# Kernel tuning notes

Hardware: AMD Instinct MI355X
Metric: run time of the kernel (lower is better)

## Reference

```python
import jax, jax.numpy as jnp
import numpy as np

HEADS = 4
DIM_HEAD = 64
SCALE = 8.0
EPS = 1e-5  # fp32 branch of the original LayerNorm


def setup_inputs() -> dict:
    key = jax.random.key(0)
    k1, k2, k3 = jax.random.split(key, 3)
    B, C, F, H, W = 2, 256, 4, 32, 32
    inner = HEADS * DIM_HEAD  # 256
    x = jax.random.normal(k1, (B, C, F, H, W), dtype=jnp.float32)
    gamma = jnp.ones((1, C, 1, 1, 1), dtype=jnp.float32)
    w_qkv = jax.random.normal(k2, (3 * inner, C), dtype=jnp.float32) * 0.05
    w_out = jax.random.normal(k3, (C, inner), dtype=jnp.float32) * 0.05
    return {"x": x, "gamma": gamma, "w_qkv": w_qkv, "w_out": w_out}


def _l2norm(t):
    return t / jnp.sqrt(jnp.sum(t * t, axis=-1, keepdims=True) + 1e-12)


def reference(x, gamma, w_qkv, w_out):
    B, C, F, H, W = x.shape
    N = F * H * W
    inner = HEADS * DIM_HEAD
    residual = x

    # channel LayerNorm (biased variance over dim=1)
    mean = jnp.mean(x, axis=1, keepdims=True)
    var = jnp.mean((x - mean) ** 2, axis=1, keepdims=True)
    xn = (x - mean) / jnp.sqrt(var + EPS) * gamma

    # 1x1x1 conv == channel matmul; flatten spatial dims to sequence
    xn_flat = xn.reshape(B, C, N)                      # [B, C, N]
    qkv = jnp.einsum('oc,bcn->bon', w_qkv, xn_flat)    # [B, 3*inner, N]
    qkv = qkv.reshape(B, 3, HEADS, DIM_HEAD, N)        # chunk then split heads
    qkv = jnp.transpose(qkv, (1, 0, 2, 4, 3))          # [3, B, h, N, d]
    q, k, v = qkv[0], qkv[1], qkv[2]

    q = _l2norm(q)
    k = _l2norm(k)

    sim = jnp.einsum('bhid,bhjd->bhij', q, k) * SCALE  # [B, h, N, N]
    attn = jax.nn.softmax(sim, axis=-1)
    out = jnp.einsum('bhij,bhjd->bhid', attn, v)       # [B, h, N, d]

    # 'b h n d -> b (h d) n' then 1x1x1 out conv
    out = jnp.transpose(out, (0, 1, 3, 2)).reshape(B, inner, N)
    out = jnp.einsum('oi,bin->bon', w_out, out).reshape(B, C, F, H, W)
    return out + residual
```

## Files before the change

kernel.cpp:

```cpp
#include <hip/hip_runtime.h>

#define BATCH 2
#define CCH   256
#define NSEQ  4096
#define NH    4
#define DH    64
#define INNER 256

typedef __attribute__((ext_vector_type(8))) __bf16 bf16x8;
typedef __attribute__((ext_vector_type(4))) float f32x4;
typedef __attribute__((ext_vector_type(8))) unsigned short u16x8;
typedef __attribute__((ext_vector_type(4))) unsigned short u16x4;

#define GLD16(gsrc, ldst)                                                     \
  __builtin_amdgcn_global_load_lds(                                           \
      (const __attribute__((address_space(1))) unsigned int*)(const void*)(gsrc), \
      (__attribute__((address_space(3))) unsigned int*)(void*)(ldst), 16, 0, 0)

static __device__ __forceinline__ unsigned short f2bfr(float f) {
  union { float f; unsigned u; } v; v.f = f;
  return (unsigned short)((v.u + 0x8000u) >> 16);
}
static __device__ __forceinline__ unsigned pack2(float f0, float f1) {
  union { float f; unsigned u; } a, b; a.f = f0; b.f = f1;
  return __builtin_amdgcn_perm(b.u + 0x8000u, a.u + 0x8000u, 0x07060302u);
}
static __device__ __forceinline__ unsigned cvtpk(float lo, float hi) {
  unsigned r;
  asm("v_cvt_pk_bf16_f32 %0, %1, %2" : "=v"(r) : "v"(lo), "v"(hi));
  return r;
}
static __device__ __forceinline__ float bf2f(unsigned short u) {
  union { unsigned u; float f; } v; v.u = ((unsigned)u) << 16;
  return v.f;
}
static __device__ __forceinline__ bf16x8 ldb(const unsigned short* p) {
  return *(const bf16x8*)p;
}
static __device__ __forceinline__ f32x4 mm(bf16x8 a, bf16x8 b, f32x4 c) {
  return __builtin_amdgcn_mfma_f32_16x16x32_bf16(a, b, c, 0, 0, 0);
}
static __device__ __forceinline__ float ex2(float x) {
  return __builtin_amdgcn_exp2f(x);
}

__global__ __launch_bounds__(256) void k_lncvt(const float* __restrict__ x,
                                               const float* __restrict__ gamma,
                                               unsigned short* __restrict__ xn,
                                               const float* __restrict__ wq,
                                               const float* __restrict__ wo,
                                               unsigned short* __restrict__ wqb,
                                               unsigned short* __restrict__ wob) {
  int blk = blockIdx.x;
  if (blk >= 256) {
    int t = (blk - 256) * 256 + threadIdx.x;
    int e = t * 4;
    if (e < 768 * 256) {
      float4 v = *(const float4*)(wq + e);
      u16x4 pk = { f2bfr(v.x), f2bfr(v.y), f2bfr(v.z), f2bfr(v.w) };
      *(u16x4*)(wqb + e) = pk;
    } else {
      int e2 = e - 768 * 256;
      float4 v = *(const float4*)(wo + e2);
      u16x4 pk = { f2bfr(v.x), f2bfr(v.y), f2bfr(v.z), f2bfr(v.w) };
      *(u16x4*)(wob + e2) = pk;
    }
    return;
  }
  int b  = blk >> 7;
  int n0 = (blk & 127) * 32;
  int t  = threadIdx.x;
  int nl = t & 31;
  int cg = t >> 5;
  int n  = n0 + nl;
  const float* xp = x + ((size_t)(b * CCH + cg * 32)) * NSEQ + n;
  float vals[32];
  float s = 0.f, s2 = 0.f;
#pragma unroll
  for (int j = 0; j < 32; j++) {
    float v = xp[(size_t)j * NSEQ];
    vals[j] = v; s += v; s2 += v * v;
  }
  __shared__ float rs[8][32], rs2[8][32];
  rs[cg][nl] = s; rs2[cg][nl] = s2;
  __syncthreads();
  float S = 0.f, S2 = 0.f;
#pragma unroll
  for (int g = 0; g < 8; g++) { S += rs[g][nl]; S2 += rs2[g][nl]; }
  float mean = S * (1.f / 256.f);
  float var  = S2 * (1.f / 256.f) - mean * mean;
  float rstd = rsqrtf(var + 1e-5f);
  unsigned short* dst = xn + ((size_t)b * NSEQ + n) * CCH + cg * 32;
#pragma unroll
  for (int j0 = 0; j0 < 32; j0 += 8) {
    u16x8 pk;
#pragma unroll
    for (int j = 0; j < 8; j++)
      pk[j] = f2bfr((vals[j0 + j] - mean) * rstd * gamma[cg * 32 + j0 + j]);
    *(u16x8*)(dst + j0) = pk;
  }
}

__global__ __launch_bounds__(256) void k_qkv(const unsigned short* __restrict__ wqb,
                                             const unsigned short* __restrict__ xn,
                                             unsigned short* __restrict__ qkv,
                                             unsigned short* __restrict__ qt,
                                             unsigned short* __restrict__ ktb) {
  int n0 = blockIdx.x * 64;
  int oi = blockIdx.y;
  int o0 = oi * 64;
  int b  = blockIdx.z;
  __shared__ unsigned short Al[64 * 256];
  __shared__ unsigned short Bl[64 * 256];
  int t = threadIdx.x;
  int lane = t & 63, w = t >> 6;
  int c = lane & 15, quad = lane >> 4;
  int wm = w >> 1, wn = w & 1;
  f32x4 acc[2][2] = {};
  int lr2 = lane >> 5;
  int lch = lane & 31;
  const unsigned short* apg = wqb + (size_t)o0 * CCH;
  const unsigned short* bpg = xn + ((size_t)b * NSEQ + n0) * CCH;
#pragma unroll
  for (int q = 0; q < 8; q++) {
    int r = w * 16 + q * 2 + lr2;
    int srcoff = r * CCH + ((lch ^ (r & 7)) * 8);
    GLD16(apg + srcoff, Al + (size_t)(w * 16 + q * 2) * 256);
    GLD16(bpg + srcoff, Bl + (size_t)(w * 16 + q * 2) * 256);
  }
  __syncthreads();
#pragma unroll
  for (int ks = 0; ks < 8; ks++) {
    int ra0 = wm * 32 + c, ra1 = ra0 + 16;
    int rb0 = wn * 32 + c, rb1 = rb0 + 16;
    bf16x8 a0 = ldb(&Al[ra0 * 256 + (((ks * 4 + quad) ^ (ra0 & 7)) * 8)]);
    bf16x8 a1 = ldb(&Al[ra1 * 256 + (((ks * 4 + quad) ^ (ra1 & 7)) * 8)]);
    bf16x8 b0 = ldb(&Bl[rb0 * 256 + (((ks * 4 + quad) ^ (rb0 & 7)) * 8)]);
    bf16x8 b1 = ldb(&Bl[rb1 * 256 + (((ks * 4 + quad) ^ (rb1 & 7)) * 8)]);
    acc[0][0] = mm(a0, b0, acc[0][0]);
    acc[0][1] = mm(a0, b1, acc[0][1]);
    acc[1][0] = mm(a1, b0, acc[1][0]);
    acc[1][1] = mm(a1, b1, acc[1][1]);
  }
  if (oi < 8) {
    float* sq = (float*)Al;
    float s0 = 0.f, s1 = 0.f;
#pragma unroll
    for (int i = 0; i < 2; i++)
#pragma unroll
      for (int rr = 0; rr < 4; rr++) {
        s0 += acc[i][0][rr] * acc[i][0][rr];
        s1 += acc[i][1][rr] * acc[i][1][rr];
      }
    s0 += __shfl_xor(s0, 16); s0 += __shfl_xor(s0, 32);
    s1 += __shfl_xor(s1, 16); s1 += __shfl_xor(s1, 32);
    __syncthreads();
    if (quad == 0) {
      sq[wm * 64 + wn * 32 + c]      = s0;
      sq[wm * 64 + wn * 32 + 16 + c] = s1;
    }
    __syncthreads();
    float r0 = rsqrtf(sq[wn * 32 + c]      + sq[64 + wn * 32 + c]      + 1e-12f);
    float r1 = rsqrtf(sq[wn * 32 + 16 + c] + sq[64 + wn * 32 + 16 + c] + 1e-12f);
    if (oi < 4) { r0 *= 11.541560327111707f; r1 *= 11.541560327111707f; }
    int h = oi & 3;
    unsigned short* base = (oi < 4 ? qt : ktb) + ((size_t)(b * NH + h) * NSEQ) * DH;
#pragma unroll
    for (int i = 0; i < 2; i++)
#pragma unroll
      for (int j = 0; j < 2; j++) {
        float rsc = j ? r1 : r0;
        int n = n0 + wn * 32 + j * 16 + c;
        int d = wm * 32 + i * 16 + quad * 4;
        uint2 pk = { pack2(acc[i][j][0] * rsc, acc[i][j][1] * rsc),
                     pack2(acc[i][j][2] * rsc, acc[i][j][3] * rsc) };
        *(uint2*)(base + (size_t)n * DH + d) = pk;
      }
  } else {
#pragma unroll
    for (int i = 0; i < 2; i++)
#pragma unroll
      for (int j = 0; j < 2; j++)
#pragma unroll
        for (int rr = 0; rr < 4; rr++) {
          int o = o0 + wm * 32 + i * 16 + quad * 4 + rr;
          int n = n0 + wn * 32 + j * 16 + c;
          qkv[((size_t)b * 768 + o) * NSEQ + n] = f2bfr(acc[i][j][rr]);
        }
  }
}

__global__ __launch_bounds__(256, 4) void k_attn(
    const unsigned short* __restrict__ qt,
    const unsigned short* __restrict__ ktb,
    const unsigned short* __restrict__ qkv,
    unsigned short* __restrict__ opart,
    float* __restrict__ lpart,
    int S, int kvlen) {
  int i0 = blockIdx.x * 128;
  int h  = blockIdx.y;
  int bz = blockIdx.z;
  int b  = bz / S, s = bz % S;
  __shared__ unsigned short Kl[64 * 64];
  __shared__ unsigned short Vl[2][64 * 64];
  __shared__ unsigned short Pl[128 * 64];
  int t = threadIdx.x;
  int lane = t & 63, w = t >> 6;
  int c = lane & 15, quad = lane >> 4;

  const unsigned short* qbase = qt  + ((size_t)(b * NH + h) * NSEQ) * DH;
  const unsigned short* kbase = ktb + ((size_t)(b * NH + h) * NSEQ) * DH;
  const unsigned short* vbase = qkv + ((size_t)b * 768 + 512 + h * 64) * NSEQ;

  int rlo = w * 32 + c, rhi = rlo + 16;
  const unsigned short* qlo = qbase + (size_t)(i0 + rlo) * DH + quad * 8;
  const unsigned short* qhi = qlo + 16 * DH;
  bf16x8 qlo0 = ldb(qlo), qlo1 = ldb(qlo + 32);
  bf16x8 qhi0 = ldb(qhi), qhi1 = ldb(qhi + 32);

  u16x8 onesu;
#pragma unroll
  for (int j = 0; j < 8; j++) onesu[j] = 0x3F80;
  bf16x8 ones = *(bf16x8*)&onesu;

  f32x4 acclo[4] = {}, acchi[4] = {};
  f32x4 accllo = {}, acclhi = {};

  int slr = lane >> 3, slc = lane & 7;
  int ssw = (slc ^ slr) * 8;
  const unsigned short* kp = kbase + (size_t)(s * kvlen + w * 16 + slr) * DH + ssw;
  const unsigned short* vp = vbase + (size_t)(w * 16 + slr) * NSEQ + s * kvlen + ssw;
  int sw0 = (quad ^ (c & 7)) * 8;
  int sw1 = sw0 ^ 32;
  int r7 = rlo & 7;

  int nIt = kvlen / 64;
  GLD16(kp,            &Kl[(w * 16)     * 64]);
  GLD16(kp + 8 * DH,   &Kl[(w * 16 + 8) * 64]);
  GLD16(vp,            &Vl[0][(w * 16)     * 64]);
  GLD16(vp + 8 * NSEQ, &Vl[0][(w * 16 + 8) * 64]);
  kp += 64 * DH; vp += 64;

  for (int it = 0; it < nIt; it++) {
    int cur = it & 1;
    __syncthreads();
    if (it + 1 < nIt) {
      int nb = cur ^ 1;
      GLD16(vp,            &Vl[nb][(w * 16)     * 64]);
      GLD16(vp + 8 * NSEQ, &Vl[nb][(w * 16 + 8) * 64]);
      vp += 64;
    }

#pragma unroll
    for (int jt = 0; jt < 4; jt++) {
      bf16x8 k0 = ldb(&Kl[(jt * 16 + c) * 64 + sw0]);
      bf16x8 k1 = ldb(&Kl[(jt * 16 + c) * 64 + sw1]);
      __builtin_amdgcn_s_setprio(1);
      f32x4 zl = {}; zl = mm(k0, qlo0, zl); zl = mm(k1, qlo1, zl);
      f32x4 zh = {}; zh = mm(k0, qhi0, zh); zh = mm(k1, qhi1, zh);
      __builtin_amdgcn_s_setprio(0);
      int cj = jt * 2 + (quad >> 1);
      int sub = (quad & 1) * 4;
      uint2 pkl = { cvtpk(ex2(zl[0]), ex2(zl[1])),
                    cvtpk(ex2(zl[2]), ex2(zl[3])) };
      *(uint2*)&Pl[rlo * 64 + ((cj ^ r7) * 8) + sub] = pkl;
      uint2 pkh = { cvtpk(ex2(zh[0]), ex2(zh[1])),
                    cvtpk(ex2(zh[2]), ex2(zh[3])) };
      *(uint2*)&Pl[rhi * 64 + ((cj ^ r7) * 8) + sub] = pkh;
    }
    bf16x8 plo0 = ldb(&Pl[rlo * 64 + ((quad ^ r7) * 8)]);
    bf16x8 plo1 = ldb(&Pl[rlo * 64 + (((quad + 4) ^ r7) * 8)]);
    bf16x8 phi0 = ldb(&Pl[rhi * 64 + ((quad ^ r7) * 8)]);
    bf16x8 phi1 = ldb(&Pl[rhi * 64 + (((quad + 4) ^ r7) * 8)]);

    if (it + 1 < nIt) {
      __builtin_amdgcn_sched_barrier(0);
      __builtin_amdgcn_s_barrier();
      __builtin_amdgcn_sched_barrier(0);
      GLD16(kp,          &Kl[(w * 16)     * 64]);
      GLD16(kp + 8 * DH, &Kl[(w * 16 + 8) * 64]);
      kp += 64 * DH;
    }

#pragma unroll
    for (int dt = 0; dt < 4; dt++) {
      bf16x8 v0 = ldb(&Vl[cur][(dt * 16 + c) * 64 + sw0]);
      bf16x8 v1 = ldb(&Vl[cur][(dt * 16 + c) * 64 + sw1]);
      __builtin_amdgcn_s_setprio(1);
      acclo[dt] = mm(plo0, v0, acclo[dt]);
      acclo[dt] = mm(plo1, v1, acclo[dt]);
      acchi[dt] = mm(phi0, v0, acchi[dt]);
      acchi[dt] = mm(phi1, v1, acchi[dt]);
      __builtin_amdgcn_s_setprio(0);
    }
    __builtin_amdgcn_s_setprio(1);
    accllo = mm(plo0, ones, accllo); accllo = mm(plo1, ones, accllo);
    acclhi = mm(phi0, ones, acclhi); acclhi = mm(phi1, ones, acclhi);
    __builtin_amdgcn_s_setprio(0);
  }

  size_t rb = ((size_t)(b * NH + h) * S + s) * NSEQ + i0 + w * 32;
  if (c == 0) {
#pragma unroll
    for (int rr = 0; rr < 4; rr++) {
      lpart[rb + quad * 4 + rr]      = accllo[rr];
      lpart[rb + 16 + quad * 4 + rr] = acclhi[rr];
    }
  }
#pragma unroll
  for (int rr = 0; rr < 4; rr++)
#pragma unroll
    for (int dt = 0; dt < 4; dt++) {
      opart[(rb + quad * 4 + rr) * 64 + dt * 16 + c]      = f2bfr(acclo[dt][rr]);
      opart[(rb + 16 + quad * 4 + rr) * 64 + dt * 16 + c] = f2bfr(acchi[dt][rr]);
    }
}

__global__ __launch_bounds__(256) void k_merge(
    const unsigned short* __restrict__ opart,
    const float* __restrict__ lpart,
    unsigned short* __restrict__ ao, int S) {
  int t = blockIdx.x * 256 + threadIdx.x;
  int row = t >> 2;
  int dseg = (t & 3) * 16;
  int b = row >> 14, rem = row & 16383;
  int h = rem >> 12, i = rem & 4095;

  float l = 0.f;
  float o[16];
#pragma unroll
  for (int j = 0; j < 16; j++) o[j] = 0.f;
  for (int s = 0; s < S; s++) {
    size_t rb = ((size_t)(b * NH + h) * S + s) * NSEQ + i;
    l += lpart[rb];
    const unsigned short* p = opart + rb * 64 + dseg;
    u16x8 v0 = *(const u16x8*)p;
    u16x8 v1 = *(const u16x8*)(p + 8);
#pragma unroll
    for (int j = 0; j < 8; j++) {
      o[j]     += bf2f(v0[j]);
      o[8 + j] += bf2f(v1[j]);
    }
  }
  float inv = 1.f / l;
  unsigned short* dst = ao + ((size_t)b * NSEQ + i) * INNER + h * 64 + dseg;
  uint4 pk0 = { pack2(o[0] * inv, o[1] * inv),  pack2(o[2] * inv, o[3] * inv),
                pack2(o[4] * inv, o[5] * inv),  pack2(o[6] * inv, o[7] * inv) };
  uint4 pk1 = { pack2(o[8] * inv, o[9] * inv),  pack2(o[10] * inv, o[11] * inv),
                pack2(o[12] * inv, o[13] * inv),pack2(o[14] * inv, o[15] * inv) };
  *(uint4*)dst = pk0;
  *(uint4*)(dst + 8) = pk1;
}

__global__ __launch_bounds__(256) void k_out(const unsigned short* __restrict__ wob,
                                             const unsigned short* __restrict__ ao,
                                             const float* __restrict__ x,
                                             float* __restrict__ out) {
  int n0 = blockIdx.x * 64;
  int o0 = blockIdx.y * 64;
  int b  = blockIdx.z;
  __shared__ unsigned short Al[64 * 256];
  __shared__ unsigned short Bl[64 * 256];
  int t = threadIdx.x;
  int lane = t & 63, w = t >> 6;
  int c = lane & 15, quad = lane >> 4;
  int wm = w >> 1, wn = w & 1;
  f32x4 acc[2][2] = {};
  int lr2 = lane >> 5;
  int lch = lane & 31;
  const unsigned short* apg = wob + (size_t)o0 * INNER;
  const unsigned short* bpg = ao + ((size_t)b * NSEQ + n0) * INNER;
#pragma unroll
  for (int q = 0; q < 8; q++) {
    int r = w * 16 + q * 2 + lr2;
    int srcoff = r * INNER + ((lch ^ (r & 7)) * 8);
    GLD16(apg + srcoff, Al + (size_t)(w * 16 + q * 2) * 256);
    GLD16(bpg + srcoff, Bl + (size_t)(w * 16 + q * 2) * 256);
  }
  __syncthreads();
#pragma unroll
  for (int ks = 0; ks < 8; ks++) {
    int ra0 = wm * 32 + c, ra1 = ra0 + 16;
    int rb0 = wn * 32 + c, rb1 = rb0 + 16;
    bf16x8 a0 = ldb(&Al[ra0 * 256 + (((ks * 4 + quad) ^ (ra0 & 7)) * 8)]);
    bf16x8 a1 = ldb(&Al[ra1 * 256 + (((ks * 4 + quad) ^ (ra1 & 7)) * 8)]);
    bf16x8 b0 = ldb(&Bl[rb0 * 256 + (((ks * 4 + quad) ^ (rb0 & 7)) * 8)]);
    bf16x8 b1 = ldb(&Bl[rb1 * 256 + (((ks * 4 + quad) ^ (rb1 & 7)) * 8)]);
    acc[0][0] = mm(a0, b0, acc[0][0]);
    acc[0][1] = mm(a0, b1, acc[0][1]);
    acc[1][0] = mm(a1, b0, acc[1][0]);
    acc[1][1] = mm(a1, b1, acc[1][1]);
  }
#pragma unroll
  for (int i = 0; i < 2; i++)
#pragma unroll
    for (int j = 0; j < 2; j++)
#pragma unroll
      for (int rr = 0; rr < 4; rr++) {
        int o = o0 + wm * 32 + i * 16 + quad * 4 + rr;
        int n = n0 + wn * 32 + j * 16 + c;
        size_t idx = ((size_t)b * CCH + o) * NSEQ + n;
        out[idx] = acc[i][j][rr] + x[idx];
      }
}

extern "C" void kernel_launch(void* const* d_in, const int* in_sizes, int n_in,
                              void* d_out, int out_size, void* d_ws, size_t ws_size,
                              hipStream_t stream) {
  const float* x     = (const float*)d_in[0];
  const float* gamma = (const float*)d_in[1];
  const float* wq    = (const float*)d_in[2];
  const float* wo    = (const float*)d_in[3];
  float* out = (float*)d_out;

  const size_t MB = 1u << 20;
  char* ws = (char*)d_ws;
  unsigned short* ao  = (unsigned short*)ws;
  unsigned short* xn  = (unsigned short*)(ws + 4 * MB);
  unsigned short* qkv = (unsigned short*)(ws + 8 * MB);
  unsigned short* wqb = (unsigned short*)(ws + 20 * MB);
  unsigned short* wob = (unsigned short*)(ws + 20 * MB + 512 * 1024);
  unsigned short* qt  = (unsigned short*)(ws + 21 * MB);
  unsigned short* ktb = (unsigned short*)(ws + 25 * MB);
  unsigned short* opart = (unsigned short*)(ws + 29 * MB);
  int S;
  if (ws_size >= 48 * MB) S = 4;
  else if (ws_size >= 40 * MB) S = 2;
  else S = 1;
  size_t opart_bytes = (size_t)S * BATCH * NH * NSEQ * DH * 2;
  float* lpart = (float*)(ws + 29 * MB + opart_bytes);
  int kvlen = NSEQ / S;

  k_lncvt<<<dim3(512),          256, 0, stream>>>(x, gamma, xn, wq, wo, wqb, wob);
  k_qkv  <<<dim3(64, 12, 2),    256, 0, stream>>>(wqb, xn, qkv, qt, ktb);
  k_attn <<<dim3(32, 4, 2 * S), 256, 0, stream>>>(qt, ktb, qkv, opart,
                                                  lpart, S, kvlen);
  k_merge<<<dim3(512),          256, 0, stream>>>(opart, lpart, ao, S);
  k_out  <<<dim3(64, 4, 2),     256, 0, stream>>>(wob, ao, x, out);
}
```

Before: 128.9 us.

## Keep attention probabilities in registers by permuting K rows to match MFMA layout

The attention kernel now loads K tiles straight from global memory into registers, using a permuted row mapping so the QK^T MFMA output lands in the operand layout the PV MFMA needs. This removes the shared-memory P buffer, its round trip, the K shared tile and one block barrier per iteration. In exchange every wave loads K from global memory itself with no sharing in LDS, which adds global/L2 traffic and raises register pressure.

```diff
diff --git a/kernel.cpp b/kernel.cpp
--- a/kernel.cpp
+++ b/kernel.cpp
@@ -201,9 +201,7 @@
   int h  = blockIdx.y;
   int bz = blockIdx.z;
   int b  = bz / S, s = bz % S;
-  __shared__ unsigned short Kl[64 * 64];
   __shared__ unsigned short Vl[2][64 * 64];
-  __shared__ unsigned short Pl[128 * 64];
   int t = threadIdx.x;
   int lane = t & 63, w = t >> 6;
   int c = lane & 15, quad = lane >> 4;
@@ -228,18 +226,21 @@
 
   int slr = lane >> 3, slc = lane & 7;
   int ssw = (slc ^ slr) * 8;
-  const unsigned short* kp = kbase + (size_t)(s * kvlen + w * 16 + slr) * DH + ssw;
   const unsigned short* vp = vbase + (size_t)(w * 16 + slr) * NSEQ + s * kvlen + ssw;
   int sw0 = (quad ^ (c & 7)) * 8;
   int sw1 = sw0 ^ 32;
-  int r7 = rlo & 7;
+
+  const unsigned short* kp0 =
+      kbase + (size_t)(s * kvlen + (c >> 2) * 8 + (c & 3)) * DH + quad * 8;
 
   int nIt = kvlen / 64;
-  GLD16(kp,            &Kl[(w * 16)     * 64]);
-  GLD16(kp + 8 * DH,   &Kl[(w * 16 + 8) * 64]);
   GLD16(vp,            &Vl[0][(w * 16)     * 64]);
   GLD16(vp + 8 * NSEQ, &Vl[0][(w * 16 + 8) * 64]);
-  kp += 64 * DH; vp += 64;
+  vp += 64;
+  bf16x8 k00 = ldb(kp0),          k01 = ldb(kp0 + 32);
+  bf16x8 k10 = ldb(kp0 + 4 * DH), k11 = ldb(kp0 + 4 * DH + 32);
+
+  union U4 { unsigned u[4]; bf16x8 v; };
 
   for (int it = 0; it < nIt; it++) {
     int cur = it & 1;
@@ -250,36 +251,48 @@
       GLD16(vp + 8 * NSEQ, &Vl[nb][(w * 16 + 8) * 64]);
       vp += 64;
     }
-
-#pragma unroll
-    for (int jt = 0; jt < 4; jt++) {
-      bf16x8 k0 = ldb(&Kl[(jt * 16 + c) * 64 + sw0]);
-      bf16x8 k1 = ldb(&Kl[(jt * 16 + c) * 64 + sw1]);
+    const unsigned short* kq = kp0 + 32 * DH;
+    bf16x8 k20 = ldb(kq),          k21 = ldb(kq + 32);
+    bf16x8 k30 = ldb(kq + 4 * DH), k31 = ldb(kq + 4 * DH + 32);
+
+    U4 plo0, plo1, phi0, phi1;
+    {
       __builtin_amdgcn_s_setprio(1);
-      f32x4 zl = {}; zl = mm(k0, qlo0, zl); zl = mm(k1, qlo1, zl);
-      f32x4 zh = {}; zh = mm(k0, qhi0, zh); zh = mm(k1, qhi1, zh);
+      f32x4 zl0 = {}; zl0 = mm(k00, qlo0, zl0); zl0 = mm(k01, qlo1, zl0);
+      f32x4 zh0 = {}; zh0 = mm(k00, qhi0, zh0); zh0 = mm(k01, qhi1, zh0);
+      f32x4 zl1 = {}; zl1 = mm(k10, qlo0, zl1); zl1 = mm(k11, qlo1, zl1);
+      f32x4 zh1 = {}; zh1 = mm(k10, qhi0, zh1); zh1 = mm(k11, qhi1, zh1);
       __builtin_amdgcn_s_setprio(0);
-      int cj = jt * 2 + (quad >> 1);
-      int sub = (quad & 1) * 4;
-      uint2 pkl = { cvtpk(ex2(zl[0]), ex2(zl[1])),
-                    cvtpk(ex2(zl[2]), ex2(zl[3])) };
-      *(uint2*)&Pl[rlo * 64 + ((cj ^ r7) * 8) + sub] = pkl;
-      uint2 pkh = { cvtpk(ex2(zh[0]), ex2(zh[1])),
-                    cvtpk(ex2(zh[2]), ex2(zh[3])) };
-      *(uint2*)&Pl[rhi * 64 + ((cj ^ r7) * 8) + sub] = pkh;
-    }
-    bf16x8 plo0 = ldb(&Pl[rlo * 64 + ((quad ^ r7) * 8)]);
-    bf16x8 plo1 = ldb(&Pl[rlo * 64 + (((quad + 4) ^ r7) * 8)]);
-    bf16x8 phi0 = ldb(&Pl[rhi * 64 + ((quad ^ r7) * 8)]);
-    bf16x8 phi1 = ldb(&Pl[rhi * 64 + (((quad + 4) ^ r7) * 8)]);
+      plo0.u[0] = cvtpk(ex2(zl0[0]), ex2(zl0[1]));
+      plo0.u[1] = cvtpk(ex2(zl0[2]), ex2(zl0[3]));
+      plo0.u[2] = cvtpk(ex2(zl1[0]), ex2(zl1[1]));
+      plo0.u[3] = cvtpk(ex2(zl1[2]), ex2(zl1[3]));
+      phi0.u[0] = cvtpk(ex2(zh0[0]), ex2(zh0[1]));
+      phi0.u[1] = cvtpk(ex2(zh0[2]), ex2(zh0[3]));
+      phi0.u[2] = cvtpk(ex2(zh1[0]), ex2(zh1[1]));
+      phi0.u[3] = cvtpk(ex2(zh1[2]), ex2(zh1[3]));
+    }
+    {
+      __builtin_amdgcn_s_setprio(1);
+      f32x4 zl2 = {}; zl2 = mm(k20, qlo0, zl2); zl2 = mm(k21, qlo1, zl2);
+      f32x4 zh2 = {}; zh2 = mm(k20, qhi0, zh2); zh2 = mm(k21, qhi1, zh2);
+      f32x4 zl3 = {}; zl3 = mm(k30, qlo0, zl3); zl3 = mm(k31, qlo1, zl3);
+      f32x4 zh3 = {}; zh3 = mm(k30, qhi0, zh3); zh3 = mm(k31, qhi1, zh3);
+      __builtin_amdgcn_s_setprio(0);
+      plo1.u[0] = cvtpk(ex2(zl2[0]), ex2(zl2[1]));
+      plo1.u[1] = cvtpk(ex2(zl2[2]), ex2(zl2[3]));
+      plo1.u[2] = cvtpk(ex2(zl3[0]), ex2(zl3[1]));
+      plo1.u[3] = cvtpk(ex2(zl3[2]), ex2(zl3[3]));
+      phi1.u[0] = cvtpk(ex2(zh2[0]), ex2(zh2[1]));
+      phi1.u[1] = cvtpk(ex2(zh2[2]), ex2(zh2[3]));
+      phi1.u[2] = cvtpk(ex2(zh3[0]), ex2(zh3[1]));
+      phi1.u[3] = cvtpk(ex2(zh3[2]), ex2(zh3[3]));
+    }
 
     if (it + 1 < nIt) {
-      __builtin_amdgcn_sched_barrier(0);
-      __builtin_amdgcn_s_barrier();
-      __builtin_amdgcn_sched_barrier(0);
-      GLD16(kp,          &Kl[(w * 16)     * 64]);
-      GLD16(kp + 8 * DH, &Kl[(w * 16 + 8) * 64]);
-      kp += 64 * DH;
+      kp0 += 64 * DH;
+      k00 = ldb(kp0);          k01 = ldb(kp0 + 32);
+      k10 = ldb(kp0 + 4 * DH); k11 = ldb(kp0 + 4 * DH + 32);
     }
 
 #pragma unroll
@@ -287,15 +300,15 @@
       bf16x8 v0 = ldb(&Vl[cur][(dt * 16 + c) * 64 + sw0]);
       bf16x8 v1 = ldb(&Vl[cur][(dt * 16 + c) * 64 + sw1]);
       __builtin_amdgcn_s_setprio(1);
-      acclo[dt] = mm(plo0, v0, acclo[dt]);
-      acclo[dt] = mm(plo1, v1, acclo[dt]);
-      acchi[dt] = mm(phi0, v0, acchi[dt]);
-      acchi[dt] = mm(phi1, v1, acchi[dt]);
+      acclo[dt] = mm(plo0.v, v0, acclo[dt]);
+      acclo[dt] = mm(plo1.v, v1, acclo[dt]);
+      acchi[dt] = mm(phi0.v, v0, acchi[dt]);
+      acchi[dt] = mm(phi1.v, v1, acchi[dt]);
       __builtin_amdgcn_s_setprio(0);
     }
     __builtin_amdgcn_s_setprio(1);
-    accllo = mm(plo0, ones, accllo); accllo = mm(plo1, ones, accllo);
-    acclhi = mm(phi0, ones, acclhi); acclhi = mm(phi1, ones, acclhi);
+    accllo = mm(plo0.v, ones, accllo); accllo = mm(plo1.v, ones, accllo);
+    acclhi = mm(phi0.v, ones, acclhi); acclhi = mm(phi1.v, ones, acclhi);
     __builtin_amdgcn_s_setprio(0);
   }
 
```

New measurement: 156.4 us. +21.4%, slower.
